# Optimization experiments

Hardware: AMD Instinct MI355X
Metric: run time of the kernel (lower is better)

The kernel has to match this reference:

```python
import jax, jax.numpy as jnp
import numpy as np


def _layernorm(x, g, b, eps=1e-5):
    mu = jnp.mean(x, axis=-1, keepdims=True)
    var = jnp.mean((x - mu) ** 2, axis=-1, keepdims=True)
    return g * (x - mu) * jax.lax.rsqrt(var + eps) + b


def _pos_encoding(S, D, dtype):
    # standard sinusoidal positional encoding [S, D]
    pos = jnp.arange(S, dtype=jnp.float32)[:, None]
    i = jnp.arange(0, D, 2, dtype=jnp.float32)[None, :]
    ang = pos / jnp.power(10000.0, i / D)
    return jnp.stack([jnp.sin(ang), jnp.cos(ang)], axis=-1).reshape(S, D).astype(dtype)


def _mha(x, theta, Wc, bc, num_heads):
    # Quantum projection: per-wire RX(x)+RX(theta) from |0>, <Z> = cos(x+theta).
    # The module uses ONE shared q_layer for q, k, v, so q == k == v.
    B, S, D = x.shape
    dk = D // num_heads
    p = jnp.cos(x + theta)                                    # [B,S,D]
    ph = p.reshape(B, S, num_heads, dk)                        # [B,S,H,dk]
    scale = 1.0 / jnp.sqrt(jnp.asarray(dk, x.dtype))
    scores = jnp.einsum('bqhd,bkhd->bhqk', ph, ph) * scale     # [B,H,S,S]
    attn = jax.nn.softmax(scores, axis=-1)
    out = jnp.einsum('bhqk,bkhd->bqhd', attn, ph).reshape(B, S, D)
    return out @ Wc + bc


def _ffn(x, theta, W1, b1, W2, b2):
    # RY-encoder + trainable RY per wire -> <Z> = cos(x + theta)
    h = jnp.cos(x + theta)
    h = h @ W1 + b1
    return jax.nn.relu(h) @ W2 + b2


def _forward(tokens, embedding, theta_attn, Wc, bc, ln1_g, ln1_b, theta_ffn,
             W1, b1, W2, b2, ln2_g, ln2_b, Wcls, bcls, num_heads):
    x = embedding[tokens]                                      # [B,S,D]
    B, S, D = x.shape
    x = x + _pos_encoding(S, D, x.dtype)
    n_blocks = theta_attn.shape[0]
    for l in range(n_blocks):  # small fixed layer count
        a = _mha(x, theta_attn[l], Wc[l], bc[l], num_heads)
        x = _layernorm(x + a, ln1_g[l], ln1_b[l])
        f = _ffn(x, theta_ffn[l], W1[l], b1[l], W2[l], b2[l])
        x = _layernorm(x + f, ln2_g[l], ln2_b[l])
    pooled = jnp.mean(x, axis=1)                               # [B,D]
    return pooled @ Wcls + bcls                                # [B,C]


def setup_inputs() -> dict:
    key = jax.random.key(0)
    ks = jax.random.split(key, 8)
    V, D, L, F, C = 32000, 512, 2, 2048, 10
    B, S = 8, 1024
    s = 0.02
    return {
        'tokens': jax.random.randint(ks[0], (B, S), 0, V, dtype=jnp.int32),
        'embedding': jax.random.normal(ks[1], (V, D), jnp.float32) * s,
        'theta_attn': jax.random.normal(ks[2], (L, D), jnp.float32) * s,
        'Wc': jax.random.normal(ks[3], (L, D, D), jnp.float32) * s,
        'bc': jnp.zeros((L, D), jnp.float32),
        'ln1_g': jnp.ones((L, D), jnp.float32),
        'ln1_b': jnp.zeros((L, D), jnp.float32),
        'theta_ffn': jax.random.normal(ks[4], (L, D), jnp.float32) * s,
        'W1': jax.random.normal(ks[5], (L, D, F), jnp.float32) * s,
        'b1': jnp.zeros((L, F), jnp.float32),
        'W2': jax.random.normal(ks[6], (L, F, D), jnp.float32) * s,
        'b2': jnp.zeros((L, D), jnp.float32),
        'ln2_g': jnp.ones((L, D), jnp.float32),
        'ln2_b': jnp.zeros((L, D), jnp.float32),
        'Wcls': jax.random.normal(ks[7], (D, C), jnp.float32) * s,
        'bcls': jnp.zeros((C,), jnp.float32),
        'num_heads': 8,
    }


def reference(tokens, embedding, theta_attn, Wc, bc, ln1_g, ln1_b, theta_ffn,
              W1, b1, W2, b2, ln2_g, ln2_b, Wcls, bcls, num_heads):
    return _forward(tokens, embedding, theta_attn, Wc, bc, ln1_g, ln1_b,
                    theta_ffn, W1, b1, W2, b2, ln2_g, ln2_b, Wcls, bcls, num_heads)
```

## Files before the change

### kernel.cpp

```cpp
#include <hip/hip_runtime.h>
#include <math.h>

#define BB 8
#define SS 1024
#define DD 512
#define HH 8
#define DK 64
#define FF 2048
#define NCLS 10
#define ROWS (BB*SS)
#define NLAYERS 2

typedef short bf16x8 __attribute__((ext_vector_type(8)));
typedef float f32x4 __attribute__((ext_vector_type(4)));

__device__ inline short f2bf(float f) {
    unsigned u = __float_as_uint(f);
    u += 0x7FFF + ((u >> 16) & 1);
    return (short)(u >> 16);
}

__device__ inline void gload_lds16(const void* g, void* l) {
    __builtin_amdgcn_global_load_lds((const __attribute__((address_space(1))) void*)g,
                                     (__attribute__((address_space(3))) void*)l, 16, 0, 0);
}

__global__ __launch_bounds__(128) void k_embed_pe(const int* __restrict__ tokens,
                                                  const float* __restrict__ emb,
                                                  float* __restrict__ x) {
    int row = blockIdx.x;
    int s = row & (SS - 1);
    int tok = tokens[row];
    const float4* e = reinterpret_cast<const float4*>(emb + (size_t)tok * DD);
    float4 v = e[threadIdx.x];
    float pe[4];
#pragma unroll
    for (int j = 0; j < 4; ++j) {
        int d = threadIdx.x * 4 + j;
        int jj = d >> 1;
        float inv = expf(-((float)(2 * jj) / (float)DD) * 9.210340371976184f);
        float ang = (float)s * inv;
        pe[j] = (d & 1) ? cosf(ang) : sinf(ang);
    }
    v.x += pe[0]; v.y += pe[1]; v.z += pe[2]; v.w += pe[3];
    reinterpret_cast<float4*>(x + (size_t)row * DD)[threadIdx.x] = v;
}

template <int WT>
__global__ __launch_bounds__(256) void k_cosp(const float* __restrict__ x,
                                              const float* __restrict__ theta,
                                              short* __restrict__ p,
                                              short* __restrict__ pt) {
    int d0 = blockIdx.x * 64, s0 = blockIdx.y * 64, b = blockIdx.z;
    int t = threadIdx.x;
    int tc = t & 15, tr = t >> 4;
    __shared__ short lt[64][68];
    float4 th = *reinterpret_cast<const float4*>(theta + d0 + tc * 4);
#pragma unroll
    for (int i = 0; i < 4; ++i) {
        int s = tr + 16 * i;
        float4 xv = *reinterpret_cast<const float4*>(
            x + ((size_t)b * SS + s0 + s) * DD + d0 + tc * 4);
        short4 o;
        o.x = f2bf(cosf(xv.x + th.x));
        o.y = f2bf(cosf(xv.y + th.y));
        o.z = f2bf(cosf(xv.z + th.z));
        o.w = f2bf(cosf(xv.w + th.w));
        *reinterpret_cast<short4*>(p + ((size_t)b * SS + s0 + s) * DD + d0 + tc * 4) = o;
        if (WT) {
            lt[tc * 4 + 0][s] = o.x;
            lt[tc * 4 + 1][s] = o.y;
            lt[tc * 4 + 2][s] = o.z;
            lt[tc * 4 + 3][s] = o.w;
        }
    }
    if (WT) {
        __syncthreads();
#pragma unroll
        for (int i = 0; i < 4; ++i) {
            int d = tr + 16 * i;
            short4 v;
            v.x = lt[d][tc * 4 + 0];
            v.y = lt[d][tc * 4 + 1];
            v.z = lt[d][tc * 4 + 2];
            v.w = lt[d][tc * 4 + 3];
            *reinterpret_cast<short4*>(pt + ((size_t)b * DD + d0 + d) * SS + s0 + tc * 4) = v;
        }
    }
}

__global__ __launch_bounds__(256) void k_wtrans(const float* __restrict__ W,
                                                short* __restrict__ Wt,
                                                int K, int N) {
    __shared__ float tile[32][33];
    int n0 = blockIdx.x * 32, k0 = blockIdx.y * 32;
    int tx = threadIdx.x & 31, ty = threadIdx.x >> 5;
#pragma unroll
    for (int i = 0; i < 4; ++i)
        tile[ty + 8 * i][tx] = W[(size_t)(k0 + ty + 8 * i) * N + n0 + tx];
    __syncthreads();
#pragma unroll
    for (int i = 0; i < 4; ++i)
        Wt[(size_t)(n0 + ty + 8 * i) * K + k0 + tx] = f2bf(tile[tx][ty + 8 * i]);
}

#define KVB 64
#define NT (SS / KVB)
__global__ __launch_bounds__(256) void k_attn(const short* __restrict__ p,
                                              const short* __restrict__ pt,
                                              short* __restrict__ aout) {
    int bid = blockIdx.x;
    int qc = bid >> 6, bh = bid & 63;
    int b = bh >> 3, h = bh & 7;
    int t = threadIdx.x, w = t >> 6, l = t & 63;
    int lg = l >> 4, lr = l & 15;

    __shared__ __attribute__((aligned(16))) short Kt[3][KVB * 64];
    __shared__ __attribute__((aligned(16))) short Vt[3][64 * KVB];
    __shared__ __attribute__((aligned(16))) short Pl[4][16 * 72];

    bf16x8 qf[2][2];
#pragma unroll
    for (int s = 0; s < 2; ++s) {
        size_t prow = ((size_t)b * SS + qc * 128 + w * 32 + s * 16 + lr) * DD + h * DK;
        qf[s][0] = *reinterpret_cast<const bf16x8*>(p + prow + lg * 8);
        qf[s][1] = *reinterpret_cast<const bf16x8*>(p + prow + 32 + lg * 8);
    }

    f32x4 acc[2][4];
#pragma unroll
    for (int s = 0; s < 2; ++s)
#pragma unroll
        for (int dt = 0; dt < 4; ++dt) acc[s][dt] = (f32x4){0.f, 0.f, 0.f, 0.f};
    float denom[2] = {0.f, 0.f};

    const short* pK = p + (size_t)b * SS * DD + h * DK;
    const short* pV = pt + ((size_t)b * DD + h * DK) * SS;
    short* myP = &Pl[w][0];

#define STAGE_ATT(bi, kk0)                                                      \
    {                                                                           \
        _Pragma("unroll")                                                       \
        for (int i = 0; i < 2; ++i) {                                           \
            int c = i * 256 + t;                                                \
            int row = c >> 3, sl = c & 7, ssl = sl ^ (row & 7);                 \
            gload_lds16(pK + (size_t)((kk0) + row) * DD + ssl * 8,              \
                        &Kt[bi][0] + (size_t)(i * 256 + w * 64) * 8);           \
            gload_lds16(pV + (size_t)row * SS + (kk0) + ssl * 8,                \
                        &Vt[bi][0] + (size_t)(i * 256 + w * 64) * 8);           \
        }                                                                       \
    }

    STAGE_ATT(0, 0);
    STAGE_ATT(1, KVB);

    for (int kt3 = 0; kt3 < NT; ++kt3) {
        if (kt3 + 1 < NT)
            asm volatile("s_waitcnt vmcnt(4)\n\ts_barrier" ::: "memory");
        else
            asm volatile("s_waitcnt vmcnt(0)\n\ts_barrier" ::: "memory");
        if (kt3 + 2 < NT) STAGE_ATT((kt3 + 2) % 3, (kt3 + 2) * KVB);

        const short* kb = &Kt[kt3 % 3][0];
        const short* vb = &Vt[kt3 % 3][0];

#pragma unroll
        for (int s = 0; s < 2; ++s) {
            f32x4 sc[4];
            __builtin_amdgcn_s_setprio(1);
#pragma unroll
            for (int kt = 0; kt < 4; ++kt) {
                int row = kt * 16 + lr;
                bf16x8 ka0 = *reinterpret_cast<const bf16x8*>(kb + row * 64 + ((lg ^ (row & 7)) * 8));
                bf16x8 ka1 = *reinterpret_cast<const bf16x8*>(kb + row * 64 + (((lg + 4) ^ (row & 7)) * 8));
                f32x4 z = (f32x4){0.f, 0.f, 0.f, 0.f};
                z = __builtin_amdgcn_mfma_f32_16x16x32_bf16(ka0, qf[s][0], z, 0, 0, 0);
                z = __builtin_amdgcn_mfma_f32_16x16x32_bf16(ka1, qf[s][1], z, 0, 0, 0);
                sc[kt] = z;
            }
            __builtin_amdgcn_s_setprio(0);
#pragma unroll
            for (int kt = 0; kt < 4; ++kt) {
                float e0 = __expf(sc[kt].x * 0.125f);
                float e1 = __expf(sc[kt].y * 0.125f);
                float e2 = __expf(sc[kt].z * 0.125f);
                float e3 = __expf(sc[kt].w * 0.125f);
                denom[s] += (e0 + e1) + (e2 + e3);
                short4 pk;
                pk.x = f2bf(e0); pk.y = f2bf(e1); pk.z = f2bf(e2); pk.w = f2bf(e3);
                *reinterpret_cast<short4*>(myP + lr * 72 + kt * 16 + lg * 4) = pk;
            }
            asm volatile("s_waitcnt lgkmcnt(0)" ::: "memory");
            __builtin_amdgcn_s_setprio(1);
#pragma unroll
            for (int kt2 = 0; kt2 < 2; ++kt2) {
                bf16x8 pb = *reinterpret_cast<const bf16x8*>(myP + lr * 72 + kt2 * 32 + lg * 8);
#pragma unroll
                for (int dt = 0; dt < 4; ++dt) {
                    int row = dt * 16 + lr;
                    bf16x8 va = *reinterpret_cast<const bf16x8*>(
                        vb + row * 64 + (((kt2 * 4 + lg) ^ (row & 7)) * 8));
                    acc[s][dt] = __builtin_amdgcn_mfma_f32_16x16x32_bf16(va, pb, acc[s][dt], 0, 0, 0);
                }
            }
            __builtin_amdgcn_s_setprio(0);
        }
    }
#undef STAGE_ATT

#pragma unroll
    for (int s = 0; s < 2; ++s) {
        float d2 = denom[s];
        d2 += __shfl_xor(d2, 16);
        d2 += __shfl_xor(d2, 32);
        float inv = 1.0f / d2;
        size_t orow = ((size_t)b * SS + qc * 128 + w * 32 + s * 16 + lr) * DD + h * DK;
#pragma unroll
        for (int dt = 0; dt < 4; ++dt) {
            short4 o;
            o.x = f2bf(acc[s][dt].x * inv);
            o.y = f2bf(acc[s][dt].y * inv);
            o.z = f2bf(acc[s][dt].z * inv);
            o.w = f2bf(acc[s][dt].w * inv);
            *reinterpret_cast<short4*>(aout + orow + dt * 16 + lg * 4) = o;
        }
    }
}

template <int RELU, int OUTBF>
__global__ __launch_bounds__(256) void k_mm(const short* __restrict__ A,
                                            const short* __restrict__ Bt,
                                            const float* __restrict__ bias,
                                            void* __restrict__ C,
                                            int N, int K, int gx) {
    __shared__ __attribute__((aligned(16))) short Al[4][128 * 32];
    __shared__ __attribute__((aligned(16))) short Bl[4][128 * 32];
    int t = threadIdx.x, w = t >> 6, l = t & 63;
    int lg = l >> 4, lr = l & 15;
    int wm = w >> 1, wn = w & 1;

    int nwg = gridDim.x;
    int bid = blockIdx.x;
    int swz = (bid & 7) * (nwg >> 3) + (bid >> 3);
    int bx = swz % gx, by = swz / gx;
    int row0 = by * 128, col0 = bx * 128;

    f32x4 acc[4][4];
#pragma unroll
    for (int m = 0; m < 4; ++m)
#pragma unroll
        for (int n = 0; n < 4; ++n) acc[m][n] = (f32x4){0.f, 0.f, 0.f, 0.f};

#define STAGE_MM(buf, kk0)                                                      \
    {                                                                           \
        _Pragma("unroll")                                                       \
        for (int i = 0; i < 2; ++i) {                                           \
            int c = i * 256 + t;                                                \
            int row = c >> 2, sl = c & 3, ssl = sl ^ ((row >> 1) & 3);          \
            gload_lds16(A + (size_t)(row0 + row) * K + (kk0) + ssl * 8,         \
                        &Al[buf][0] + (size_t)(i * 256 + w * 64) * 8);          \
            gload_lds16(Bt + (size_t)(col0 + row) * K + (kk0) + ssl * 8,        \
                        &Bl[buf][0] + (size_t)(i * 256 + w * 64) * 8);          \
        }                                                                       \
    }

    const int nk = K >> 5;
    STAGE_MM(0, 0);
    if (nk > 1) STAGE_MM(1, 32);
    if (nk > 2) STAGE_MM(2, 64);

    for (int kt = 0; kt < nk; ++kt) {
        if (kt + 2 < nk)
            asm volatile("s_waitcnt vmcnt(8)\n\ts_barrier" ::: "memory");
        else if (kt + 1 < nk)
            asm volatile("s_waitcnt vmcnt(4)\n\ts_barrier" ::: "memory");
        else
            asm volatile("s_waitcnt vmcnt(0)\n\ts_barrier" ::: "memory");

        const short* a_ = &Al[kt & 3][0];
        const short* b_ = &Bl[kt & 3][0];
        bf16x8 af[4], bfr[4];
#pragma unroll
        for (int m = 0; m < 4; ++m) {
            int row = wm * 64 + m * 16 + lr;
            af[m] = *reinterpret_cast<const bf16x8*>(a_ + row * 32 + ((lg ^ ((row >> 1) & 3)) * 8));
        }
#pragma unroll
        for (int n = 0; n < 4; ++n) {
            int row = wn * 64 + n * 16 + lr;
            bfr[n] = *reinterpret_cast<const bf16x8*>(b_ + row * 32 + ((lg ^ ((row >> 1) & 3)) * 8));
        }
        if (kt + 3 < nk) STAGE_MM((kt + 3) & 3, (kt + 3) * 32);

#pragma unroll
        for (int m = 0; m < 4; ++m)
#pragma unroll
            for (int n = 0; n < 4; ++n)
                acc[m][n] = __builtin_amdgcn_mfma_f32_16x16x32_bf16(af[m], bfr[n], acc[m][n], 0, 0, 0);
    }
#undef STAGE_MM

    float bv[4];
#pragma unroll
    for (int n = 0; n < 4; ++n) bv[n] = bias[col0 + wn * 64 + n * 16 + lr];

#pragma unroll
    for (int m = 0; m < 4; ++m) {
#pragma unroll
        for (int n = 0; n < 4; ++n) {
            int col = col0 + wn * 64 + n * 16 + lr;
#pragma unroll
            for (int j = 0; j < 4; ++j) {
                int row = row0 + wm * 64 + m * 16 + lg * 4 + j;
                float v = acc[m][n][j] + bv[n];
                if (RELU) v = fmaxf(v, 0.f);
                if (OUTBF) ((short*)C)[(size_t)row * N + col] = f2bf(v);
                else       ((float*)C)[(size_t)row * N + col] = v;
            }
        }
    }
}

template <int COSP>
__global__ __launch_bounds__(128) void k_add_ln(float* __restrict__ x,
                                                const float* __restrict__ rr,
                                                const float* __restrict__ g,
                                                const float* __restrict__ bb,
                                                const float* __restrict__ theta,
                                                short* __restrict__ p) {
    int row = blockIdx.x;
    int t = threadIdx.x;
    float4 v = *reinterpret_cast<const float4*>(x + (size_t)row * DD + t * 4);
    float4 av = *reinterpret_cast<const float4*>(rr + (size_t)row * DD + t * 4);
    v.x += av.x; v.y += av.y; v.z += av.z; v.w += av.w;
    float s = v.x + v.y + v.z + v.w;
    float s2 = v.x * v.x + v.y * v.y + v.z * v.z + v.w * v.w;
#pragma unroll
    for (int off = 32; off > 0; off >>= 1) {
        s += __shfl_down(s, off);
        s2 += __shfl_down(s2, off);
    }
    __shared__ float ls[2], ls2[2];
    if ((t & 63) == 0) { ls[t >> 6] = s; ls2[t >> 6] = s2; }
    __syncthreads();
    float S1 = ls[0] + ls[1];
    float S2 = ls2[0] + ls2[1];
    float mu = S1 * (1.0f / DD);
    float var = S2 * (1.0f / DD) - mu * mu;
    float rstd = rsqrtf(var + 1e-5f);
    float4 gv = *reinterpret_cast<const float4*>(g + t * 4);
    float4 bv = *reinterpret_cast<const float4*>(bb + t * 4);
    float4 o;
    o.x = gv.x * (v.x - mu) * rstd + bv.x;
    o.y = gv.y * (v.y - mu) * rstd + bv.y;
    o.z = gv.z * (v.z - mu) * rstd + bv.z;
    o.w = gv.w * (v.w - mu) * rstd + bv.w;
    *reinterpret_cast<float4*>(x + (size_t)row * DD + t * 4) = o;
    if (COSP) {
        float4 th = *reinterpret_cast<const float4*>(theta + t * 4);
        short4 pk;
        pk.x = f2bf(cosf(o.x + th.x));
        pk.y = f2bf(cosf(o.y + th.y));
        pk.z = f2bf(cosf(o.z + th.z));
        pk.w = f2bf(cosf(o.w + th.w));
        *reinterpret_cast<short4*>(p + (size_t)row * DD + t * 4) = pk;
    }
}

__global__ __launch_bounds__(128) void k_pool(const float* __restrict__ x,
                                              float* __restrict__ part) {
    int b = blockIdx.x, c = blockIdx.y;
    int t = threadIdx.x;
    float4 s = {0.f, 0.f, 0.f, 0.f};
    for (int i = 0; i < 32; ++i) {
        float4 v = reinterpret_cast<const float4*>(
            x + ((size_t)b * SS + c * 32 + i) * DD)[t];
        s.x += v.x; s.y += v.y; s.z += v.z; s.w += v.w;
    }
    reinterpret_cast<float4*>(part + ((size_t)b * 32 + c) * DD)[t] = s;
}

__global__ __launch_bounds__(512) void k_cls(const float* __restrict__ part,
                                             const float* __restrict__ Wcls,
                                             const float* __restrict__ bcls,
                                             float* __restrict__ out) {
    int b = blockIdx.x;
    int t = threadIdx.x;
    float s = 0.f;
    for (int i = 0; i < 32; ++i) s += part[((size_t)b * 32 + i) * DD + t];
    float pooled = s * (1.0f / SS);
    float acc[NCLS];
#pragma unroll
    for (int c = 0; c < NCLS; ++c) acc[c] = pooled * Wcls[t * NCLS + c];
#pragma unroll
    for (int off = 32; off > 0; off >>= 1)
#pragma unroll
        for (int c = 0; c < NCLS; ++c) acc[c] += __shfl_xor(acc[c], off);
    __shared__ float wp[8][NCLS];
    int w = t >> 6, l = t & 63;
    if (l == 0)
#pragma unroll
        for (int c = 0; c < NCLS; ++c) wp[w][c] = acc[c];
    __syncthreads();
    if (t < NCLS) {
        float o = bcls[t];
#pragma unroll
        for (int i = 0; i < 8; ++i) o += wp[i][t];
        out[b * NCLS + t] = o;
    }
}

extern "C" void kernel_launch(void* const* d_in, const int* in_sizes, int n_in,
                              void* d_out, int out_size, void* d_ws, size_t ws_size,
                              hipStream_t stream) {
    const int* tokens      = (const int*)d_in[0];
    const float* emb       = (const float*)d_in[1];
    const float* theta_att = (const float*)d_in[2];
    const float* Wc        = (const float*)d_in[3];
    const float* bc        = (const float*)d_in[4];
    const float* ln1_g     = (const float*)d_in[5];
    const float* ln1_b     = (const float*)d_in[6];
    const float* theta_ffn = (const float*)d_in[7];
    const float* W1        = (const float*)d_in[8];
    const float* b1        = (const float*)d_in[9];
    const float* W2        = (const float*)d_in[10];
    const float* b2        = (const float*)d_in[11];
    const float* ln2_g     = (const float*)d_in[12];
    const float* ln2_b     = (const float*)d_in[13];
    const float* Wcls      = (const float*)d_in[14];
    const float* bcls      = (const float*)d_in[15];
    float* out = (float*)d_out;

    char* wsb = (char*)d_ws;
    float* x    = (float*)(wsb);
    float* t0   = (float*)(wsb + (size_t)16 * 1048576);
    short* p    = (short*)(wsb + (size_t)32 * 1048576);
    short* pt   = (short*)(wsb + (size_t)40 * 1048576);
    short* a    = (short*)(wsb + (size_t)48 * 1048576);
    short* hh   = (short*)(wsb + (size_t)56 * 1048576);
    short* Wct  = (short*)(wsb + (size_t)88 * 1048576);
    short* W1t  = (short*)(wsb + (size_t)89 * 1048576);
    short* W2t  = (short*)(wsb + (size_t)91 * 1048576);
    float* part = (float*)(wsb + (size_t)94 * 1048576);

    k_embed_pe<<<ROWS, 128, 0, stream>>>(tokens, emb, x);

    for (int l = 0; l < NLAYERS; ++l) {
        k_wtrans<<<dim3(DD / 32, DD / 32), 256, 0, stream>>>(Wc + (size_t)l * DD * DD, Wct, DD, DD);
        k_wtrans<<<dim3(FF / 32, DD / 32), 256, 0, stream>>>(W1 + (size_t)l * DD * FF, W1t, DD, FF);
        k_wtrans<<<dim3(DD / 32, FF / 32), 256, 0, stream>>>(W2 + (size_t)l * FF * DD, W2t, FF, DD);

        k_cosp<1><<<dim3(DD / 64, SS / 64, BB), 256, 0, stream>>>(x, theta_att + l * DD, p, pt);
        k_attn<<<(SS / 128) * BB * HH, 256, 0, stream>>>(p, pt, a);
        k_mm<0, 0><<<(DD / 128) * (ROWS / 128), 256, 0, stream>>>(
            a, Wct, bc + l * DD, t0, DD, DD, DD / 128);
        k_add_ln<1><<<ROWS, 128, 0, stream>>>(x, t0, ln1_g + l * DD, ln1_b + l * DD,
                                              theta_ffn + l * DD, p);
        k_mm<1, 1><<<(FF / 128) * (ROWS / 128), 256, 0, stream>>>(
            p, W1t, b1 + l * FF, hh, FF, DD, FF / 128);
        k_mm<0, 0><<<(DD / 128) * (ROWS / 128), 256, 0, stream>>>(
            hh, W2t, b2 + l * DD, t0, DD, FF, DD / 128);
        k_add_ln<0><<<ROWS, 128, 0, stream>>>(x, t0, ln2_g + l * DD, ln2_b + l * DD,
                                              (const float*)nullptr, (short*)nullptr);
    }

    k_pool<<<dim3(BB, 32), 128, 0, stream>>>(x, part);
    k_cls<<<BB, 512, 0, stream>>>(part, Wcls, bcls, out);
}
```

Measured before the change: 418.8 us.

## Keep softmax probabilities in registers and share K/V fragments across query subtiles

The attention inner loop no longer round-trips the exponentiated scores through a per-wave LDS buffer. The score accumulator layout is fed straight into PV MFMAs by switching to the 16x16x16 bf16 instruction, whose B-operand layout matches the C output of the QK MFMA. The two query subtiles are interleaved so each K and V LDS fragment is loaded once and used for both. This removes LDS writes, reads and waitcnt stalls, but doubles the number of PV MFMA instructions, each with half the K depth, and raises register pressure.

```diff
diff --git a/kernel.cpp b/kernel.cpp
--- a/kernel.cpp
+++ b/kernel.cpp
@@ -12,6 +12,7 @@
 #define NLAYERS 2
 
 typedef short bf16x8 __attribute__((ext_vector_type(8)));
+typedef short bf16x4 __attribute__((ext_vector_type(4)));
 typedef float f32x4 __attribute__((ext_vector_type(4)));
 
 __device__ inline short f2bf(float f) {
@@ -117,7 +118,6 @@
 
     __shared__ __attribute__((aligned(16))) short Kt[3][KVB * 64];
     __shared__ __attribute__((aligned(16))) short Vt[3][64 * KVB];
-    __shared__ __attribute__((aligned(16))) short Pl[4][16 * 72];
 
     bf16x8 qf[2][2];
 #pragma unroll
@@ -136,7 +136,6 @@
 
     const short* pK = p + (size_t)b * SS * DD + h * DK;
     const short* pV = pt + ((size_t)b * DD + h * DK) * SS;
-    short* myP = &Pl[w][0];
 
 #define STAGE_ATT(bi, kk0)                                                      \
     {                                                                           \
@@ -164,47 +163,53 @@
         const short* kb = &Kt[kt3 % 3][0];
         const short* vb = &Vt[kt3 % 3][0];
 
-#pragma unroll
-        for (int s = 0; s < 2; ++s) {
-            f32x4 sc[4];
-            __builtin_amdgcn_s_setprio(1);
-#pragma unroll
-            for (int kt = 0; kt < 4; ++kt) {
-                int row = kt * 16 + lr;
-                bf16x8 ka0 = *reinterpret_cast<const bf16x8*>(kb + row * 64 + ((lg ^ (row & 7)) * 8));
-                bf16x8 ka1 = *reinterpret_cast<const bf16x8*>(kb + row * 64 + (((lg + 4) ^ (row & 7)) * 8));
+        f32x4 sc[2][4];
+        __builtin_amdgcn_s_setprio(1);
+#pragma unroll
+        for (int kt = 0; kt < 4; ++kt) {
+            int row = kt * 16 + lr;
+            bf16x8 ka0 = *reinterpret_cast<const bf16x8*>(kb + row * 64 + ((lg ^ (row & 7)) * 8));
+            bf16x8 ka1 = *reinterpret_cast<const bf16x8*>(kb + row * 64 + (((lg + 4) ^ (row & 7)) * 8));
+#pragma unroll
+            for (int s = 0; s < 2; ++s) {
                 f32x4 z = (f32x4){0.f, 0.f, 0.f, 0.f};
                 z = __builtin_amdgcn_mfma_f32_16x16x32_bf16(ka0, qf[s][0], z, 0, 0, 0);
                 z = __builtin_amdgcn_mfma_f32_16x16x32_bf16(ka1, qf[s][1], z, 0, 0, 0);
-                sc[kt] = z;
+                sc[s][kt] = z;
             }
-            __builtin_amdgcn_s_setprio(0);
+        }
+        __builtin_amdgcn_s_setprio(0);
+
+        bf16x4 pb[2][4];
+#pragma unroll
+        for (int s = 0; s < 2; ++s) {
 #pragma unroll
             for (int kt = 0; kt < 4; ++kt) {
-                float e0 = __expf(sc[kt].x * 0.125f);
-                float e1 = __expf(sc[kt].y * 0.125f);
-                float e2 = __expf(sc[kt].z * 0.125f);
-                float e3 = __expf(sc[kt].w * 0.125f);
+                float e0 = __expf(sc[s][kt].x * 0.125f);
+                float e1 = __expf(sc[s][kt].y * 0.125f);
+                float e2 = __expf(sc[s][kt].z * 0.125f);
+                float e3 = __expf(sc[s][kt].w * 0.125f);
                 denom[s] += (e0 + e1) + (e2 + e3);
-                short4 pk;
-                pk.x = f2bf(e0); pk.y = f2bf(e1); pk.z = f2bf(e2); pk.w = f2bf(e3);
-                *reinterpret_cast<short4*>(myP + lr * 72 + kt * 16 + lg * 4) = pk;
+                bf16x4 pk;
+                pk[0] = f2bf(e0); pk[1] = f2bf(e1); pk[2] = f2bf(e2); pk[3] = f2bf(e3);
+                pb[s][kt] = pk;
             }
-            asm volatile("s_waitcnt lgkmcnt(0)" ::: "memory");
-            __builtin_amdgcn_s_setprio(1);
-#pragma unroll
-            for (int kt2 = 0; kt2 < 2; ++kt2) {
-                bf16x8 pb = *reinterpret_cast<const bf16x8*>(myP + lr * 72 + kt2 * 32 + lg * 8);
-#pragma unroll
-                for (int dt = 0; dt < 4; ++dt) {
-                    int row = dt * 16 + lr;
-                    bf16x8 va = *reinterpret_cast<const bf16x8*>(
-                        vb + row * 64 + (((kt2 * 4 + lg) ^ (row & 7)) * 8));
-                    acc[s][dt] = __builtin_amdgcn_mfma_f32_16x16x32_bf16(va, pb, acc[s][dt], 0, 0, 0);
-                }
+        }
+
+        __builtin_amdgcn_s_setprio(1);
+#pragma unroll
+        for (int kt = 0; kt < 4; ++kt) {
+            int c8 = kt * 2 + (lg >> 1);
+#pragma unroll
+            for (int dt = 0; dt < 4; ++dt) {
+                int row = dt * 16 + lr;
+                bf16x4 vf = *reinterpret_cast<const bf16x4*>(
+                    vb + row * 64 + ((c8 ^ (row & 7)) * 8 + (lg & 1) * 4));
+                acc[0][dt] = __builtin_amdgcn_mfma_f32_16x16x16bf16_1k(vf, pb[0][kt], acc[0][dt], 0, 0, 0);
+                acc[1][dt] = __builtin_amdgcn_mfma_f32_16x16x16bf16_1k(vf, pb[1][kt], acc[1][dt], 0, 0, 0);
             }
-            __builtin_amdgcn_s_setprio(0);
-        }
+        }
+        __builtin_amdgcn_s_setprio(0);
     }
 #undef STAGE_ATT
 
```

Measured after the change: 422.1 us. About the same (+0.8%).
